# Kernel optimization log

Measured on AMD Instinct MI355X. Metric: run time of the kernel, lower is better.

## Reference

```python
import jax, jax.numpy as jnp
import numpy as np
import math

B, N, E, H = 2, 2048, 1024, 16
D = E // H

def setup_inputs() -> dict:
    key = jax.random.key(0)
    ks = jax.random.split(key, 9)
    s = 1.0 / math.sqrt(E)
    return {
        "x": jax.random.normal(ks[0], (B, N, E), dtype=jnp.float32),
        "Wq": jax.random.uniform(ks[1], (E, E), jnp.float32, -s, s),
        "bq": jax.random.uniform(ks[2], (E,), jnp.float32, -s, s),
        "Wk": jax.random.uniform(ks[3], (E, E), jnp.float32, -s, s),
        "bk": jax.random.uniform(ks[4], (E,), jnp.float32, -s, s),
        "Wv": jax.random.uniform(ks[5], (E, E), jnp.float32, -s, s),
        "bv": jax.random.uniform(ks[6], (E,), jnp.float32, -s, s),
        "Wo": jax.random.uniform(ks[7], (E, E), jnp.float32, -s, s),
        "bo": jax.random.uniform(ks[8], (E,), jnp.float32, -s, s),
    }

def _split_heads(t):
    # [b, n, (h d)] -> [b, h, n, d]
    b, n, _ = t.shape
    return t.reshape(b, n, H, D).transpose(0, 2, 1, 3)

def reference(x, Wq, bq, Wk, bk, Wv, bv, Wo, bo):
    q = _split_heads(x @ Wq.T + bq)
    k = _split_heads(x @ Wk.T + bk)
    v = _split_heads(x @ Wv.T + bv)
    energy = jnp.einsum('bhqd,bhkd->bhqk', q, k)
    # Faithful to source: softmax first, THEN divide by sqrt(n_embedding)
    attention = jax.nn.softmax(energy, axis=-1) / jnp.sqrt(jnp.float32(E))
    out = jnp.einsum('bhqk,bhkd->bhqd', attention, v)
    out = out.transpose(0, 2, 1, 3).reshape(x.shape[0], x.shape[1], E)
    return out @ Wo.T + bo
```

## Files before the change

kernel.cpp:

```cpp
#include <hip/hip_runtime.h>


typedef __bf16 bf16x8 __attribute__((ext_vector_type(8)));
typedef float  f32x4  __attribute__((ext_vector_type(4)));
typedef float  f32x16 __attribute__((ext_vector_type(16)));
using u16 = unsigned short;
using u32 = unsigned int;
typedef u16 u16x8 __attribute__((ext_vector_type(8)));
typedef u16 u16x4 __attribute__((ext_vector_type(4)));
typedef u32 u32x4 __attribute__((ext_vector_type(4)));

constexpr int BATCH = 2, SEQ = 2048, EMB = 1024, NH = 16, HD = 64;
constexpr int MTOT = BATCH * SEQ;
constexpr int KTOT = EMB;
constexpr int NTOT = EMB;
constexpr float LOG2E = 1.44269504088896340736f;

constexpr size_t OFF_XBF = 0;
constexpr size_t OFF_WQ  = 8u * 1024 * 1024;
constexpr size_t OFF_WK  = OFF_WQ + 2u * 1024 * 1024;
constexpr size_t OFF_WV  = OFF_WK + 2u * 1024 * 1024;
constexpr size_t OFF_WO  = OFF_WV + 2u * 1024 * 1024;
constexpr size_t OFF_Q   = OFF_WO + 2u * 1024 * 1024;
constexpr size_t OFF_K   = OFF_Q  + 8u * 1024 * 1024;
constexpr size_t OFF_VT  = OFF_K  + 8u * 1024 * 1024;

__device__ __forceinline__ u16 f2bf(float f) {
  u32 u = __builtin_bit_cast(u32, f);
  u = (u + 0x7fffu + ((u >> 16) & 1u)) >> 16;
  return (u16)u;
}

__device__ __forceinline__ bf16x8 ld_bf16x8(const u16* p) {
  return __builtin_bit_cast(bf16x8, *(const u16x8*)p);
}

__device__ __forceinline__ float fexp2(float x) {
#if __has_builtin(__builtin_amdgcn_exp2f)
  return __builtin_amdgcn_exp2f(x);
#else
  return exp2f(x);
#endif
}

__device__ __forceinline__ u32 cvtpk(float lo, float hi_) {
  u32 r;
  asm("v_cvt_pk_bf16_f32 %0, %1, %2" : "=v"(r) : "v"(lo), "v"(hi_));
  return r;
}

__device__ __forceinline__ void stage16(const void* g, void* l) {
#if __has_builtin(__builtin_amdgcn_global_load_lds)
  __builtin_amdgcn_global_load_lds(
      (__attribute__((address_space(1))) void*)const_cast<void*>(g),
      (__attribute__((address_space(3))) void*)l, 16, 0, 0);
#else
  int lane = threadIdx.x & 63;
  uint4 v = *(const uint4*)g;
  *(uint4*)((char*)l + lane * 16) = v;
#endif
}

__global__ __launch_bounds__(256) void cvt_all(
    const float* __restrict__ x, const float* __restrict__ wq,
    const float* __restrict__ wk, const float* __restrict__ wv,
    const float* __restrict__ wo, u16* __restrict__ ox, u16* __restrict__ oq,
    u16* __restrict__ okk, u16* __restrict__ ov, u16* __restrict__ oo) {
  int z = blockIdx.z;
  const float* in = (z == 0) ? x : (z == 1) ? wq : (z == 2) ? wk : (z == 3) ? wv : wo;
  u16* out = (z == 0) ? ox : (z == 1) ? oq : (z == 2) ? okk : (z == 3) ? ov : oo;
  int n4 = (z == 0) ? (MTOT * EMB / 4) : (EMB * EMB / 4);
  int i = blockIdx.x * blockDim.x + threadIdx.x;
  if (i >= n4) return;
  float4 f = ((const float4*)in)[i];
  u32 lo = (u32)f2bf(f.x) | ((u32)f2bf(f.y) << 16);
  u32 hi = (u32)f2bf(f.z) | ((u32)f2bf(f.w) << 16);
  ((uint2*)out)[i] = make_uint2(lo, hi);
}

__device__ __forceinline__ void gemm_bt_core(const u16* __restrict__ A,
                                             const u16* __restrict__ Bm,
                                             const float* __restrict__ bias,
                                             void* __restrict__ out, int mode,
                                             float oscale) {
  __shared__ __align__(16) u16 sA[128 * 32];
  __shared__ __align__(16) u16 sB[128 * 32];
  const int tid = threadIdx.x, w = tid >> 6, ln = tid & 63;
  const int wr = w >> 1, wc = w & 1, qq = ln >> 4, t = ln & 15;
  const int m0 = blockIdx.y * 128, n0 = blockIdx.x * 128;

  f32x4 acc[4][4] = {};

  for (int kt = 0; kt < KTOT; kt += 32) {
#pragma unroll
    for (int j = 0; j < 2; j++) {
      int ck = w * 128 + j * 64 + ln;
      int r = ck >> 2, c2 = ck & 3;
      stage16(&A[(size_t)(m0 + r) * KTOT + kt + c2 * 8], &sA[(w * 128 + j * 64) * 8]);
      stage16(&Bm[(size_t)(n0 + r) * KTOT + kt + c2 * 8], &sB[(w * 128 + j * 64) * 8]);
    }
    __syncthreads();

    bf16x8 av[4], bv[4];
#pragma unroll
    for (int f = 0; f < 4; f++) {
      av[f] = ld_bf16x8(&sA[(wr * 64 + f * 16 + t) * 32 + qq * 8]);
      bv[f] = ld_bf16x8(&sB[(wc * 64 + f * 16 + t) * 32 + qq * 8]);
    }
#pragma unroll
    for (int i = 0; i < 4; i++)
#pragma unroll
      for (int j = 0; j < 4; j++)
        acc[i][j] = __builtin_amdgcn_mfma_f32_16x16x32_bf16(av[i], bv[j], acc[i][j], 0, 0, 0);
    __syncthreads();
  }

#pragma unroll
  for (int fc = 0; fc < 4; fc++) {
    int n = n0 + wc * 64 + fc * 16 + t;
    float bn = bias[n];
#pragma unroll
    for (int fr = 0; fr < 4; fr++) {
#pragma unroll
      for (int i = 0; i < 4; i++) {
        int m = m0 + wr * 64 + fr * 16 + qq * 4 + i;
        float v = (acc[fr][fc][i] + bn) * oscale;
        if (mode == 2) {
          ((float*)out)[(size_t)m * NTOT + n] = v;
        } else {
          int b = m >> 11, tok = m & 2047, h = n >> 6, d = n & 63;
          u16 bf = f2bf(v);
          if (mode == 0)
            ((u16*)out)[(((size_t)(b * NH + h)) * SEQ + tok) * HD + d] = bf;
          else
            ((u16*)out)[(((size_t)(b * NH + h)) * HD + d) * SEQ + tok] = bf;
        }
      }
    }
  }
}

__global__ __launch_bounds__(256) void gemm_qkv(
    const u16* __restrict__ A, const u16* __restrict__ WQ, const u16* __restrict__ WK,
    const u16* __restrict__ WV, const float* __restrict__ bq, const float* __restrict__ bk,
    const float* __restrict__ bv, u16* Qo, u16* Ko, u16* Vo) {
  int z = blockIdx.z;
  const u16* Bm = (z == 0) ? WQ : ((z == 1) ? WK : WV);
  const float* bias = (z == 0) ? bq : ((z == 1) ? bk : bv);
  u16* out = (z == 0) ? Qo : ((z == 1) ? Ko : Vo);
  gemm_bt_core(A, Bm, bias, out, (z == 2) ? 1 : 0, (z == 0) ? LOG2E : 1.0f);
}

__global__ __launch_bounds__(256) void gemm_o(const u16* __restrict__ A,
                                              const u16* __restrict__ WO,
                                              const float* __restrict__ bo,
                                              float* __restrict__ out) {
  gemm_bt_core(A, WO, bo, out, 2, 1.0f);
}

__global__ __launch_bounds__(256) void flash_attn(const u16* __restrict__ Q,
                                                  const u16* __restrict__ Kg,
                                                  const u16* __restrict__ VT,
                                                  u16* __restrict__ O) {
  const int e = blockIdx.x;
  const int xcd = e & 7, slot = e >> 3;
  const int bh = xcd * 4 + (slot & 3);
  const int qt = slot >> 2;

  const int tid = threadIdx.x, w = tid >> 6, ln = tid & 63;
  const int c = ln & 31, hi = ln >> 5;
  const int q0 = qt * 128 + w * 32;

  const u16* Qb = Q + (size_t)bh * SEQ * HD;
  const u16* Kb = Kg + (size_t)bh * SEQ * HD;
  const u16* Vb = VT + (size_t)bh * HD * SEQ;

  __shared__ __align__(16) u16 sK[2][64 * 64];
  __shared__ __align__(16) u16 sV[2][64 * 64];

  bf16x8 qf[4];
#pragma unroll
  for (int ks = 0; ks < 4; ks++)
    qf[ks] = ld_bf16x8(&Qb[(size_t)(q0 + c) * HD + ks * 16 + hi * 8]);

  f32x16 ot[2];
  ot[0] = 0.f; ot[1] = 0.f;
  float m = -1e30f, l = 0.f;

#define STAGE(buf, kt)                                                         \
  {                                                                            \
    _Pragma("unroll") for (int j = 0; j < 2; j++) {                            \
      int ck = w * 128 + j * 64 + ln;                                          \
      int r = ck >> 3, c2 = ck & 7, c2s = c2 ^ (r & 7);                        \
      stage16(&Kb[(size_t)((kt) + r) * HD + c2s * 8],                          \
              &sK[buf][(size_t)(w * 128 + j * 64) * 8]);                       \
      stage16(&Vb[(size_t)r * SEQ + (kt) + c2s * 8],                           \
              &sV[buf][(size_t)(w * 128 + j * 64) * 8]);                       \
    }                                                                          \
  }

  STAGE(0, 0)
  __syncthreads();

  int it = 0;
  for (int kt = 0; kt < SEQ; kt += 64, it ^= 1) {
    if (kt + 64 < SEQ) STAGE(it ^ 1, kt + 64)
    const u16* kbuf = sK[it];
    const u16* vbuf = sV[it];

    f32x16 st[2];
    st[0] = 0.f; st[1] = 0.f;
#pragma unroll
    for (int kb = 0; kb < 2; kb++) {
#pragma unroll
      for (int ks = 0; ks < 4; ks++) {
        int row = kb * 32 + c;
        int boff = ((2 * ks + hi) ^ (row & 7)) << 4;
        bf16x8 kf = ld_bf16x8((const u16*)((const char*)(kbuf + row * 64) + boff));
        st[kb] = __builtin_amdgcn_mfma_f32_32x32x16_bf16(kf, qf[ks], st[kb], 0, 0, 0);
      }
    }

    float t16[16];
#pragma unroll
    for (int i = 0; i < 16; i++) t16[i] = fmaxf(st[0][i], st[1][i]);
#pragma unroll
    for (int s = 8; s >= 1; s >>= 1)
#pragma unroll
      for (int i = 0; i < s; i++) t16[i] = fmaxf(t16[i], t16[i + s]);
    float pmax = fmaxf(t16[0], __shfl_xor(t16[0], 32));

    if (!__all(pmax <= m + 8.0f)) {
      float mn = fmaxf(m, pmax);
      float sc = fexp2(m - mn);
      l *= sc;
#pragma unroll
      for (int i = 0; i < 16; i++) { ot[0][i] *= sc; ot[1][i] *= sc; }
      m = mn;
    }

#pragma unroll
    for (int kb = 0; kb < 2; kb++)
#pragma unroll
      for (int i = 0; i < 16; i++) st[kb][i] = fexp2(st[kb][i] - m);

    float s16[16];
#pragma unroll
    for (int i = 0; i < 16; i++) s16[i] = st[0][i] + st[1][i];
#pragma unroll
    for (int s = 8; s >= 1; s >>= 1)
#pragma unroll
      for (int i = 0; i < s; i++) s16[i] += s16[i + s];
    l += s16[0] + __shfl_xor(s16[0], 32);

    bf16x8 pb[4];
#pragma unroll
    for (int ks = 0; ks < 4; ks++) {
      const int kbb = ks >> 1;
      const int R0 = 4 * ((2 * ks) & 3);
      const int R1 = 4 * ((2 * ks + 1) & 3);
      u32 X0 = cvtpk(st[kbb][R0], st[kbb][R0 + 1]);
      u32 X1 = cvtpk(st[kbb][R0 + 2], st[kbb][R0 + 3]);
      u32 Y0 = cvtpk(st[kbb][R1], st[kbb][R1 + 1]);
      u32 Y1 = cvtpk(st[kbb][R1 + 2], st[kbb][R1 + 3]);
      u32 B0 = hi ? X0 : Y0;
      u32 B1 = hi ? X1 : Y1;
      u32 r0 = (u32)__shfl_xor((int)B0, 32);
      u32 r1 = (u32)__shfl_xor((int)B1, 32);
      u32x4 wd;
      wd.x = hi ? r0 : X0;
      wd.y = hi ? r1 : X1;
      wd.z = hi ? Y0 : r0;
      wd.w = hi ? Y1 : r1;
      pb[ks] = __builtin_bit_cast(bf16x8, wd);
    }

#pragma unroll
    for (int ks = 0; ks < 4; ks++) {
#pragma unroll
      for (int db = 0; db < 2; db++) {
        int row = db * 32 + c;
        int boff = ((2 * ks + hi) ^ (row & 7)) << 4;
        bf16x8 vf = ld_bf16x8((const u16*)((const char*)(vbuf + row * 64) + boff));
        ot[db] = __builtin_amdgcn_mfma_f32_32x32x16_bf16(vf, pb[ks], ot[db], 0, 0, 0);
      }
    }
    __syncthreads();
  }
#undef STAGE

  const int b = bh >> 4, h = bh & 15;
  const float inv = 1.0f / (l * 32.0f);
  u16* obase = O + ((size_t)(b * SEQ + q0 + c)) * EMB + h * HD;
#pragma unroll
  for (int db = 0; db < 2; db++)
#pragma unroll
    for (int g = 0; g < 4; g++) {
      u16x4 pkt;
#pragma unroll
      for (int i = 0; i < 4; i++) pkt[i] = f2bf(ot[db][g * 4 + i] * inv);
      *(u16x4*)(obase + db * 32 + g * 8 + hi * 4) = pkt;
    }
}

extern "C" void kernel_launch(void* const* d_in, const int* in_sizes, int n_in,
                              void* d_out, int out_size, void* d_ws, size_t ws_size,
                              hipStream_t stream) {
  const float* x  = (const float*)d_in[0];
  const float* Wq = (const float*)d_in[1];
  const float* bq = (const float*)d_in[2];
  const float* Wk = (const float*)d_in[3];
  const float* bk = (const float*)d_in[4];
  const float* Wv = (const float*)d_in[5];
  const float* bv = (const float*)d_in[6];
  const float* Wo = (const float*)d_in[7];
  const float* bo = (const float*)d_in[8];

  char* ws = (char*)d_ws;
  u16* xbf = (u16*)(ws + OFF_XBF);
  u16* wqb = (u16*)(ws + OFF_WQ);
  u16* wkb = (u16*)(ws + OFF_WK);
  u16* wvb = (u16*)(ws + OFF_WV);
  u16* wob = (u16*)(ws + OFF_WO);
  u16* Qw  = (u16*)(ws + OFF_Q);
  u16* Kw  = (u16*)(ws + OFF_K);
  u16* Vw  = (u16*)(ws + OFF_VT);

  cvt_all<<<dim3(MTOT * EMB / 4 / 256, 1, 5), 256, 0, stream>>>(
      x, Wq, Wk, Wv, Wo, xbf, wqb, wkb, wvb, wob);

  gemm_qkv<<<dim3(NTOT / 128, MTOT / 128, 3), 256, 0, stream>>>(
      xbf, wqb, wkb, wvb, bq, bk, bv, Qw, Kw, Vw);

  flash_attn<<<dim3(512), 256, 0, stream>>>(Qw, Kw, Vw, xbf);

  gemm_o<<<dim3(NTOT / 128, MTOT / 128), 256, 0, stream>>>(xbf, wob, bo, (float*)d_out);
}
```

Before: 135.1 us.

## Split flash-attention KV tiles across wave pairs with LDS merge, MFMA row sums

```diff
diff --git a/kernel.cpp b/kernel.cpp
--- a/kernel.cpp
+++ b/kernel.cpp
@@ -41,6 +41,12 @@
 #else
   return exp2f(x);
 #endif
+}
+
+__device__ __forceinline__ float fmax3(float a, float b, float c) {
+  float d;
+  asm("v_max3_f32 %0, %1, %2, %3" : "=v"(d) : "v"(a), "v"(b), "v"(c));
+  return d;
 }
 
 __device__ __forceinline__ u32 cvtpk(float lo, float hi_) {
@@ -107,12 +113,39 @@
       av[f] = ld_bf16x8(&sA[(wr * 64 + f * 16 + t) * 32 + qq * 8]);
       bv[f] = ld_bf16x8(&sB[(wc * 64 + f * 16 + t) * 32 + qq * 8]);
     }
-#pragma unroll
-    for (int i = 0; i < 4; i++)
-#pragma unroll
-      for (int j = 0; j < 4; j++)
-        acc[i][j] = __builtin_amdgcn_mfma_f32_16x16x32_bf16(av[i], bv[j], acc[i][j], 0, 0, 0);
+    if (mode == 1) {
+#pragma unroll
+      for (int i = 0; i < 4; i++)
+#pragma unroll
+        for (int j = 0; j < 4; j++)
+          acc[i][j] = __builtin_amdgcn_mfma_f32_16x16x32_bf16(bv[j], av[i], acc[i][j], 0, 0, 0);
+    } else {
+#pragma unroll
+      for (int i = 0; i < 4; i++)
+#pragma unroll
+        for (int j = 0; j < 4; j++)
+          acc[i][j] = __builtin_amdgcn_mfma_f32_16x16x32_bf16(av[i], bv[j], acc[i][j], 0, 0, 0);
+    }
     __syncthreads();
+  }
+
+  if (mode == 1) {
+#pragma unroll
+    for (int j = 0; j < 4; j++)
+#pragma unroll
+      for (int ii = 0; ii < 4; ii++) {
+        int n = n0 + wc * 64 + j * 16 + qq * 4 + ii;
+        float bn = bias[n];
+        int h = n >> 6, d = n & 63;
+#pragma unroll
+        for (int i = 0; i < 4; i++) {
+          int mm = m0 + wr * 64 + i * 16 + t;
+          int b = mm >> 11, tok = mm & 2047;
+          ((u16*)out)[(((size_t)(b * NH + h)) * HD + d) * SEQ + tok] =
+              f2bf(acc[i][j][ii] + bn);
+        }
+      }
+    return;
   }
 
 #pragma unroll
@@ -129,11 +162,7 @@
           ((float*)out)[(size_t)m * NTOT + n] = v;
         } else {
           int b = m >> 11, tok = m & 2047, h = n >> 6, d = n & 63;
-          u16 bf = f2bf(v);
-          if (mode == 0)
-            ((u16*)out)[(((size_t)(b * NH + h)) * SEQ + tok) * HD + d] = bf;
-          else
-            ((u16*)out)[(((size_t)(b * NH + h)) * HD + d) * SEQ + tok] = bf;
+          ((u16*)out)[(((size_t)(b * NH + h)) * SEQ + tok) * HD + d] = f2bf(v);
         }
       }
     }
@@ -158,10 +187,10 @@
   gemm_bt_core(A, WO, bo, out, 2, 1.0f);
 }
 
-__global__ __launch_bounds__(256) void flash_attn(const u16* __restrict__ Q,
-                                                  const u16* __restrict__ Kg,
-                                                  const u16* __restrict__ VT,
-                                                  u16* __restrict__ O) {
+__global__ __launch_bounds__(512, 4) void flash_attn(const u16* __restrict__ Q,
+                                                     const u16* __restrict__ Kg,
+                                                     const u16* __restrict__ VT,
+                                                     u16* __restrict__ O) {
   const int e = blockIdx.x;
   const int xcd = e & 7, slot = e >> 3;
   const int bh = xcd * 4 + (slot & 3);
@@ -169,7 +198,8 @@
 
   const int tid = threadIdx.x, w = tid >> 6, ln = tid & 63;
   const int c = ln & 31, hi = ln >> 5;
-  const int q0 = qt * 128 + w * 32;
+  const int kb = w >> 2;
+  const int q0 = qt * 128 + (w & 3) * 32;
 
   const u16* Qb = Q + (size_t)bh * SEQ * HD;
   const u16* Kb = Kg + (size_t)bh * SEQ * HD;
@@ -177,26 +207,29 @@
 
   __shared__ __align__(16) u16 sK[2][64 * 64];
   __shared__ __align__(16) u16 sV[2][64 * 64];
+  __shared__ float2 sml[8][64];
 
   bf16x8 qf[4];
 #pragma unroll
   for (int ks = 0; ks < 4; ks++)
     qf[ks] = ld_bf16x8(&Qb[(size_t)(q0 + c) * HD + ks * 16 + hi * 8]);
 
+  const bf16x8 ones = __builtin_bit_cast(
+      bf16x8, (u16x8){0x3f80, 0x3f80, 0x3f80, 0x3f80, 0x3f80, 0x3f80, 0x3f80, 0x3f80});
+
   f32x16 ot[2];
   ot[0] = 0.f; ot[1] = 0.f;
-  float m = -1e30f, l = 0.f;
+  f32x16 acc_l = 0.f;
+  float m = -1e30f;
 
 #define STAGE(buf, kt)                                                         \
   {                                                                            \
-    _Pragma("unroll") for (int j = 0; j < 2; j++) {                            \
-      int ck = w * 128 + j * 64 + ln;                                          \
-      int r = ck >> 3, c2 = ck & 7, c2s = c2 ^ (r & 7);                        \
-      stage16(&Kb[(size_t)((kt) + r) * HD + c2s * 8],                          \
-              &sK[buf][(size_t)(w * 128 + j * 64) * 8]);                       \
-      stage16(&Vb[(size_t)r * SEQ + (kt) + c2s * 8],                           \
-              &sV[buf][(size_t)(w * 128 + j * 64) * 8]);                       \
-    }                                                                          \
+    int ck = w * 64 + ln;                                                      \
+    int r = ck >> 3, c2 = ck & 7, c2s = c2 ^ (r & 7);                          \
+    stage16(&Kb[(size_t)((kt) + r) * HD + c2s * 8],                            \
+            &sK[buf][(size_t)(w * 64) * 8]);                                   \
+    stage16(&Vb[(size_t)r * SEQ + (kt) + c2s * 8],                             \
+            &sV[buf][(size_t)(w * 64) * 8]);                                   \
   }
 
   STAGE(0, 0)
@@ -208,99 +241,101 @@
     const u16* kbuf = sK[it];
     const u16* vbuf = sV[it];
 
-    f32x16 st[2];
-    st[0] = 0.f; st[1] = 0.f;
-#pragma unroll
-    for (int kb = 0; kb < 2; kb++) {
-#pragma unroll
-      for (int ks = 0; ks < 4; ks++) {
-        int row = kb * 32 + c;
-        int boff = ((2 * ks + hi) ^ (row & 7)) << 4;
-        bf16x8 kf = ld_bf16x8((const u16*)((const char*)(kbuf + row * 64) + boff));
-        st[kb] = __builtin_amdgcn_mfma_f32_32x32x16_bf16(kf, qf[ks], st[kb], 0, 0, 0);
-      }
-    }
-
-    float t16[16];
-#pragma unroll
-    for (int i = 0; i < 16; i++) t16[i] = fmaxf(st[0][i], st[1][i]);
-#pragma unroll
-    for (int s = 8; s >= 1; s >>= 1)
-#pragma unroll
-      for (int i = 0; i < s; i++) t16[i] = fmaxf(t16[i], t16[i + s]);
-    float pmax = fmaxf(t16[0], __shfl_xor(t16[0], 32));
+    f32x16 st = 0.f;
+    __builtin_amdgcn_s_setprio(1);
+#pragma unroll
+    for (int ks = 0; ks < 4; ks++) {
+      int row = kb * 32 + c;
+      int boff = ((2 * ks + hi) ^ (row & 7)) << 4;
+      bf16x8 kf = ld_bf16x8((const u16*)((const char*)(kbuf + row * 64) + boff));
+      st = __builtin_amdgcn_mfma_f32_32x32x16_bf16(kf, qf[ks], st, 0, 0, 0);
+    }
+    __builtin_amdgcn_s_setprio(0);
+
+    float a0 = fmax3(st[0], st[1], st[2]);
+    float a1 = fmax3(st[3], st[4], st[5]);
+    float a2 = fmax3(st[6], st[7], st[8]);
+    float a3 = fmax3(st[9], st[10], st[11]);
+    float a4 = fmax3(st[12], st[13], st[14]);
+    float a5 = fmaxf(st[15], a0);
+    float b0 = fmax3(a1, a2, a3);
+    float b1 = fmax3(a4, a5, b0);
+    float pmax = fmaxf(b1, __shfl_xor(b1, 32));
 
     if (!__all(pmax <= m + 8.0f)) {
       float mn = fmaxf(m, pmax);
       float sc = fexp2(m - mn);
-      l *= sc;
+      acc_l[0] *= sc;
 #pragma unroll
       for (int i = 0; i < 16; i++) { ot[0][i] *= sc; ot[1][i] *= sc; }
       m = mn;
     }
 
 #pragma unroll
-    for (int kb = 0; kb < 2; kb++)
-#pragma unroll
-      for (int i = 0; i < 16; i++) st[kb][i] = fexp2(st[kb][i] - m);
-
-    float s16[16];
-#pragma unroll
-    for (int i = 0; i < 16; i++) s16[i] = st[0][i] + st[1][i];
-#pragma unroll
-    for (int s = 8; s >= 1; s >>= 1)
-#pragma unroll
-      for (int i = 0; i < s; i++) s16[i] += s16[i + s];
-    l += s16[0] + __shfl_xor(s16[0], 32);
-
-    bf16x8 pb[4];
-#pragma unroll
-    for (int ks = 0; ks < 4; ks++) {
-      const int kbb = ks >> 1;
-      const int R0 = 4 * ((2 * ks) & 3);
-      const int R1 = 4 * ((2 * ks + 1) & 3);
-      u32 X0 = cvtpk(st[kbb][R0], st[kbb][R0 + 1]);
-      u32 X1 = cvtpk(st[kbb][R0 + 2], st[kbb][R0 + 3]);
-      u32 Y0 = cvtpk(st[kbb][R1], st[kbb][R1 + 1]);
-      u32 Y1 = cvtpk(st[kbb][R1 + 2], st[kbb][R1 + 3]);
-      u32 B0 = hi ? X0 : Y0;
-      u32 B1 = hi ? X1 : Y1;
-      u32 r0 = (u32)__shfl_xor((int)B0, 32);
-      u32 r1 = (u32)__shfl_xor((int)B1, 32);
-      u32x4 wd;
-      wd.x = hi ? r0 : X0;
-      wd.y = hi ? r1 : X1;
-      wd.z = hi ? Y0 : r0;
-      wd.w = hi ? Y1 : r1;
-      pb[ks] = __builtin_bit_cast(bf16x8, wd);
-    }
-
-#pragma unroll
-    for (int ks = 0; ks < 4; ks++) {
+    for (int i = 0; i < 16; i++) st[i] = fexp2(st[i] - m);
+
+    bf16x8 pb[2];
+#pragma unroll
+    for (int ks2 = 0; ks2 < 2; ks2++) {
+      const int R0 = 8 * ks2;
+      const int R1 = 4 * ((2 * ks2 + 1) & 3);
+      u32 X0 = cvtpk(st[R0], st[R0 + 1]);
+      u32 X1 = cvtpk(st[R0 + 2], st[R0 + 3]);
+      u32 Y0 = cvtpk(st[R1], st[R1 + 1]);
+      u32 Y1 = cvtpk(st[R1 + 2], st[R1 + 3]);
+      asm("v_permlane32_swap_b32 %0, %1" : "+v"(X0), "+v"(Y0));
+      asm("v_permlane32_swap_b32 %0, %1" : "+v"(X1), "+v"(Y1));
+      u32x4 wd; wd.x = X0; wd.y = X1; wd.z = Y0; wd.w = Y1;
+      pb[ks2] = __builtin_bit_cast(bf16x8, wd);
+    }
+
+    __builtin_amdgcn_s_setprio(1);
+#pragma unroll
+    for (int ks2 = 0; ks2 < 2; ks2++) {
 #pragma unroll
       for (int db = 0; db < 2; db++) {
         int row = db * 32 + c;
-        int boff = ((2 * ks + hi) ^ (row & 7)) << 4;
+        int boff = ((kb * 4 + ks2 * 2 + hi) ^ (row & 7)) << 4;
         bf16x8 vf = ld_bf16x8((const u16*)((const char*)(vbuf + row * 64) + boff));
-        ot[db] = __builtin_amdgcn_mfma_f32_32x32x16_bf16(vf, pb[ks], ot[db], 0, 0, 0);
+        ot[db] = __builtin_amdgcn_mfma_f32_32x32x16_bf16(vf, pb[ks2], ot[db], 0, 0, 0);
       }
-    }
+      acc_l = __builtin_amdgcn_mfma_f32_32x32x16_bf16(ones, pb[ks2], acc_l, 0, 0, 0);
+    }
+    __builtin_amdgcn_s_setprio(0);
     __syncthreads();
   }
 #undef STAGE
 
+  float myl = acc_l[0];
+  const int pair = w & 3;
+  float* xA = (float*)sK;
+  float* xB = (float*)sV;
+  {
+    f32x16 give = (w < 4) ? ot[1] : ot[0];
+    *(f32x16*)((w < 4 ? xA : xB) + (size_t)(pair * 64 + ln) * 16) = give;
+    sml[w][ln] = make_float2(m, myl);
+  }
+  __syncthreads();
+
+  float2 po = sml[w ^ 4][ln];
+  float M2 = fmaxf(m, po.x);
+  float s_me = fexp2(m - M2), s_po = fexp2(po.x - M2);
+  float lf = myl * s_me + po.y * s_po;
+  float inv = 1.0f / (lf * 32.0f);
+  f32x16 oth = *(const f32x16*)((w < 4 ? xB : xA) + (size_t)(pair * 64 + ln) * 16);
+  f32x16 own = (w < 4) ? ot[0] : ot[1];
+  const int db = (w < 4) ? 0 : 1;
+
   const int b = bh >> 4, h = bh & 15;
-  const float inv = 1.0f / (l * 32.0f);
   u16* obase = O + ((size_t)(b * SEQ + q0 + c)) * EMB + h * HD;
 #pragma unroll
-  for (int db = 0; db < 2; db++)
-#pragma unroll
-    for (int g = 0; g < 4; g++) {
-      u16x4 pkt;
-#pragma unroll
-      for (int i = 0; i < 4; i++) pkt[i] = f2bf(ot[db][g * 4 + i] * inv);
-      *(u16x4*)(obase + db * 32 + g * 8 + hi * 4) = pkt;
-    }
+  for (int g = 0; g < 4; g++) {
+    u16x4 pkt;
+#pragma unroll
+    for (int i = 0; i < 4; i++)
+      pkt[i] = f2bf((own[g * 4 + i] * s_me + oth[g * 4 + i] * s_po) * inv);
+    *(u16x4*)(obase + db * 32 + g * 8 + hi * 4) = pkt;
+  }
 }
 
 extern "C" void kernel_launch(void* const* d_in, const int* in_sizes, int n_in,
@@ -332,7 +367,7 @@
   gemm_qkv<<<dim3(NTOT / 128, MTOT / 128, 3), 256, 0, stream>>>(
       xbf, wqb, wkb, wvb, bq, bk, bv, Qw, Kw, Vw);
 
-  flash_attn<<<dim3(512), 256, 0, stream>>>(Qw, Kw, Vw, xbf);
+  flash_attn<<<dim3(512), 512, 0, stream>>>(Qw, Kw, Vw, xbf);
 
   gemm_o<<<dim3(NTOT / 128, MTOT / 128), 256, 0, stream>>>(xbf, wob, bo, (float*)d_out);
 }
```

Result: no change. 135.0 us (-0.1%).
